# Kernel tuning notes

Hardware: AMD Instinct MI355X
Metric: run time of the kernel (lower is better)

Reference implementation:

```python
import jax, jax.numpy as jnp
import numpy as np
import math

D_POLY = 2  # polynomial order d
N_NODES = 50000
IN_FEATS = 128
H_FEATS = 64
N_EDGES = 800000


def calc_thetas(d):
    # Beta-wavelet polynomial coefficients (ascending order), matching calculate_theta2
    thetas = []
    for i in range(d + 1):
        p = np.poly1d([1.0])
        for _ in range(i):
            p = p * np.poly1d([0.5, 0.0])      # (x/2)
        for _ in range(d - i):
            p = p * np.poly1d([-0.5, 1.0])     # (1 - x/2)
        beta = math.gamma(i + 1) * math.gamma(d + 1 - i) / math.gamma(d + 2)
        p = p / beta
        asc = p.coeffs[::-1]                   # ascending coefficients
        asc = np.concatenate([asc, np.zeros(d + 1 - len(asc))])
        thetas.append(asc.astype(np.float32))
    return thetas

THETAS = calc_thetas(D_POLY)


def setup_inputs() -> dict:
    key = jax.random.key(0)
    ks = jax.random.split(key, 7)
    features = jax.random.normal(ks[0], (N_NODES, IN_FEATS), dtype=jnp.float32)
    src = jax.random.randint(ks[1], (N_EDGES,), 0, N_NODES)
    dst = jax.random.randint(ks[2], (N_EDGES,), 0, N_NODES)
    s1 = 1.0 / math.sqrt(IN_FEATS)
    W1 = jax.random.uniform(ks[3], (H_FEATS, IN_FEATS), jnp.float32, -s1, s1)
    b1 = jnp.zeros((H_FEATS,), jnp.float32)
    s2 = 1.0 / math.sqrt(H_FEATS * (D_POLY + 1))
    W2 = jax.random.uniform(ks[4], (H_FEATS, H_FEATS * (D_POLY + 1)), jnp.float32, -s2, s2)
    b2 = jnp.zeros((H_FEATS,), jnp.float32)
    return {"features": features, "src": src, "dst": dst,
            "W1": W1, "b1": b1, "W2": W2, "b2": b2}


def reference(features, src, dst, W1, b1, W2, b2):
    N = features.shape[0]
    # linear1 + ReLU
    x = jax.nn.relu(features @ W1.T + b1)  # [N, H]
    # D^{-1/2} from in-degrees (clamped at 1)
    deg = jax.ops.segment_sum(jnp.ones_like(dst, dtype=x.dtype), dst, num_segments=N)
    D_invsqrt = jnp.clip(deg, 1.0, None) ** -0.5  # [N]
    D_invsqrt = D_invsqrt[:, None]

    def unn_laplacian(f):
        # f - D^{-1/2} A D^{-1/2} f   (aggregation onto destination nodes)
        agg = jax.ops.segment_sum((f * D_invsqrt)[src], dst, num_segments=N)
        return f - agg * D_invsqrt

    outs = []
    for theta in THETAS:
        f = x
        h = theta[0] * x
        for k in range(1, len(theta)):
            f = unn_laplacian(f)
            h = h + theta[k] * f
        outs.append(h)
    feats_final = jnp.concatenate(outs, axis=-1)  # [N, H*(d+1)]
    return feats_final @ W2.T + b2
```

## Files before the change

### kernel.cpp

```cpp
#include <hip/hip_runtime.h>

#define NN 50000
#define NE 800000
#define INF 128
#define HF 64
#define K2 192
#define MAXDEG 64

typedef __attribute__((ext_vector_type(8))) short short8;
typedef __attribute__((ext_vector_type(4))) float float4v;
typedef __attribute__((ext_vector_type(4))) unsigned short ushort4v;
typedef __attribute__((ext_vector_type(2))) unsigned int uint2v;

__device__ inline unsigned short f2bf(float x) {
    unsigned int u = __float_as_uint(x);
    u += 0x7FFFu + ((u >> 16) & 1u);
    return (unsigned short)(u >> 16);
}
__device__ inline float bflo(unsigned int p) { return __uint_as_float(p << 16); }
__device__ inline float bfhi(unsigned int p) { return __uint_as_float(p & 0xFFFF0000u); }


__global__ __launch_bounds__(256) void fill_ell_part(const int* __restrict__ src,
                                                     const int* __restrict__ dst,
                                                     int* __restrict__ cnt,
                                                     unsigned short* __restrict__ ell) {
    int chunk = blockIdx.x >> 3;
    int p     = blockIdx.x & 7;
    int e0 = (chunk * 256 + (int)threadIdx.x) * 4;
    if (e0 >= NE) return;
    int4 d4 = *reinterpret_cast<const int4*>(dst + e0);
    int dd[4] = {d4.x, d4.y, d4.z, d4.w};
#pragma unroll
    for (int j = 0; j < 4; ++j) {
        int d = dd[j];
        if (d / 6250 == p) {
            int pos = atomicAdd(&cnt[d], 1);
            if (pos < MAXDEG) ell[d * MAXDEG + pos] = (unsigned short)src[e0 + j];
        }
    }
}


__global__ void pack_b(const float* __restrict__ W1, const float* __restrict__ W2,
                       unsigned short* __restrict__ Bp1, unsigned short* __restrict__ Bp2,
                       int* __restrict__ cnt,
                       unsigned short* __restrict__ hb0, unsigned short* __restrict__ hb1) {
    int gid = blockIdx.x * 256 + threadIdx.x;
    for (int z = gid; z < NN; z += 20480) cnt[z] = 0;
    if (gid < HF) {
        hb0[(size_t)NN * HF + gid] = 0;
        hb1[(size_t)NN * HF + gid] = 0;
    }
    if (gid >= 20480) return;
    if (gid < 8192) {
        int j  = gid & 7;
        int l  = (gid >> 3) & 63;
        int nt = (gid >> 9) & 3;
        int kc = gid >> 11;
        int n = nt * 16 + (l & 15);
        int k = kc * 32 + (l >> 4) * 8 + j;
        Bp1[gid] = f2bf(W1[n * INF + k]);
    } else {
        int g = gid - 8192;
        int j  = g & 7;
        int l  = (g >> 3) & 63;
        int nt = (g >> 9) & 3;
        int kc = g >> 11;
        int n = nt * 16 + (l & 15);
        int k = kc * 32 + (l >> 4) * 8 + j;
        const float* row = W2 + (size_t)n * K2;
        float v;
        if (k < 64) {
            v = 3.0f * row[k];
        } else if (k < 128) {
            int c = k - 64;
            v = -3.0f * row[c] + 3.0f * row[64 + c];
        } else {
            int c = k - 128;
            v = 0.75f * row[c] - 1.5f * row[64 + c] + 0.75f * row[128 + c];
        }
        Bp2[g] = f2bf(v);
    }
}


__global__ __launch_bounds__(256) void gemm1_mfma(const float* __restrict__ F,
                                                  const unsigned short* __restrict__ Bp,
                                                  const float* __restrict__ b1,
                                                  const int* __restrict__ cnt,
                                                  unsigned short* __restrict__ xb,
                                                  unsigned short* __restrict__ hb0) {
    int tid  = threadIdx.x;
    int lane = tid & 63;
    int wv   = tid >> 6;
    int m0   = blockIdx.x * 64 + wv * 16;
    if (m0 >= NN) return;
    int mrow = lane & 15;
    int q    = lane >> 4;

    float4v acc[4];
#pragma unroll
    for (int nt = 0; nt < 4; ++nt) acc[nt] = (float4v){0.f, 0.f, 0.f, 0.f};

    const float* arow = F + (size_t)(m0 + mrow) * INF + q * 8;
#pragma unroll
    for (int kc = 0; kc < INF / 32; ++kc) {
        const float* ap = arow + kc * 32;
        float4v a0 = *reinterpret_cast<const float4v*>(ap);
        float4v a1 = *reinterpret_cast<const float4v*>(ap + 4);
        short8 af;
        af[0] = (short)f2bf(a0[0]); af[1] = (short)f2bf(a0[1]);
        af[2] = (short)f2bf(a0[2]); af[3] = (short)f2bf(a0[3]);
        af[4] = (short)f2bf(a1[0]); af[5] = (short)f2bf(a1[1]);
        af[6] = (short)f2bf(a1[2]); af[7] = (short)f2bf(a1[3]);
#pragma unroll
        for (int nt = 0; nt < 4; ++nt) {
            short8 bf = *reinterpret_cast<const short8*>(Bp + (((kc * 4 + nt) * 64 + lane) << 3));
            acc[nt] = __builtin_amdgcn_mfma_f32_16x16x32_bf16(af, bf, acc[nt], 0, 0, 0);
        }
    }

    float dn[4];
#pragma unroll
    for (int r = 0; r < 4; ++r) {
        int c = cnt[m0 + q * 4 + r];
        c = c > MAXDEG ? MAXDEG : c;
        dn[r] = rsqrtf((float)(c < 1 ? 1 : c));
    }

#pragma unroll
    for (int nt = 0; nt < 4; ++nt) {
        int n = nt * 16 + mrow;
        float bv = b1[n];
#pragma unroll
        for (int r = 0; r < 4; ++r) {
            int node = m0 + q * 4 + r;
            float v = acc[nt][r] + bv;
            v = v > 0.0f ? v : 0.0f;
            xb [(size_t)node * HF + n] = f2bf(v);
            hb0[(size_t)node * HF + n] = f2bf(v * dn[r]);
        }
    }
}


__device__ inline void gather_accum(const uint2v* __restrict__ hbd,
                                    int s0, int s1, int s2, int s3,
                                    int wmax, int base, int jj,
                                    float& e0, float& e1, float& e2, float& e3) {
    float a0=0,a1=0,a2=0,a3=0;
    float b0=0,b1=0,b2=0,b3=0;
    float c0=0,c1=0,c2=0,c3=0;
    float d0=0,d1=0,d2=0,d3=0;
    for (int k = 0; k < wmax; k += 8) {
        int o = base + (k >> 2);
        int t0 = __shfl(s0, o), t1 = __shfl(s1, o);
        int t2 = __shfl(s2, o), t3 = __shfl(s3, o);
        uint2v p0 = hbd[(size_t)t0 * 16 + jj];
        uint2v p1 = hbd[(size_t)t1 * 16 + jj];
        uint2v p2 = hbd[(size_t)t2 * 16 + jj];
        uint2v p3 = hbd[(size_t)t3 * 16 + jj];
        if (k + 4 < wmax) {
            int u0 = __shfl(s0, o + 1), u1 = __shfl(s1, o + 1);
            int u2 = __shfl(s2, o + 1), u3 = __shfl(s3, o + 1);
            uint2v q0 = hbd[(size_t)u0 * 16 + jj];
            uint2v q1 = hbd[(size_t)u1 * 16 + jj];
            uint2v q2 = hbd[(size_t)u2 * 16 + jj];
            uint2v q3 = hbd[(size_t)u3 * 16 + jj];
            a0 += bflo(q0[0]); a1 += bfhi(q0[0]); a2 += bflo(q0[1]); a3 += bfhi(q0[1]);
            b0 += bflo(q1[0]); b1 += bfhi(q1[0]); b2 += bflo(q1[1]); b3 += bfhi(q1[1]);
            c0 += bflo(q2[0]); c1 += bfhi(q2[0]); c2 += bflo(q2[1]); c3 += bfhi(q2[1]);
            d0 += bflo(q3[0]); d1 += bfhi(q3[0]); d2 += bflo(q3[1]); d3 += bfhi(q3[1]);
        }
        a0 += bflo(p0[0]); a1 += bfhi(p0[0]); a2 += bflo(p0[1]); a3 += bfhi(p0[1]);
        b0 += bflo(p1[0]); b1 += bfhi(p1[0]); b2 += bflo(p1[1]); b3 += bfhi(p1[1]);
        c0 += bflo(p2[0]); c1 += bfhi(p2[0]); c2 += bflo(p2[1]); c3 += bfhi(p2[1]);
        d0 += bflo(p3[0]); d1 += bfhi(p3[0]); d2 += bflo(p3[1]); d3 += bfhi(p3[1]);
    }
    e0 = (a0 + b0) + (c0 + d0);
    e1 = (a1 + b1) + (c1 + d1);
    e2 = (a2 + b2) + (c2 + d2);
    e3 = (a3 + b3) + (c3 + d3);
}


__global__ __launch_bounds__(256) void gather_quad(const unsigned short* __restrict__ ell,
                                                   const int* __restrict__ cnt,
                                                   const unsigned short* __restrict__ fin,
                                                   const unsigned short* __restrict__ hb,
                                                   unsigned short* __restrict__ fout,
                                                   unsigned short* __restrict__ hout) {
    int lane  = threadIdx.x & 63;
    int wv    = threadIdx.x >> 6;
    int which = lane >> 4;
    int jj    = lane & 15;
    int n = blockIdx.x * 16 + wv * 4 + which;
    int deg = cnt[n];
    deg = deg > MAXDEG ? MAXDEG : deg;

    ushort4v ids = *reinterpret_cast<const ushort4v*>(ell + (size_t)n * MAXDEG + jj * 4);
    int slot = jj * 4;
    int s0 = (slot + 0 < deg) ? (int)ids[0] : NN;
    int s1 = (slot + 1 < deg) ? (int)ids[1] : NN;
    int s2 = (slot + 2 < deg) ? (int)ids[2] : NN;
    int s3 = (slot + 3 < deg) ? (int)ids[3] : NN;

    int wmax = deg;
    wmax = max(wmax, __shfl_xor(wmax, 16));
    wmax = max(wmax, __shfl_xor(wmax, 32));

    float e0, e1, e2, e3;
    gather_accum((const uint2v*)hb, s0, s1, s2, s3, wmax, which * 16, jj, e0, e1, e2, e3);

    float dn = rsqrtf((float)(deg < 1 ? 1 : deg));

    uint2v xv = ((const uint2v*)fin)[(size_t)n * 16 + jj];
    float f0 = bflo(xv[0]) - e0 * dn;
    float f1 = bfhi(xv[0]) - e1 * dn;
    float f2 = bflo(xv[1]) - e2 * dn;
    float f3 = bfhi(xv[1]) - e3 * dn;
    uint2v ov;
    ov[0] = (unsigned int)f2bf(f0) | ((unsigned int)f2bf(f1) << 16);
    ov[1] = (unsigned int)f2bf(f2) | ((unsigned int)f2bf(f3) << 16);
    ((uint2v*)fout)[(size_t)n * 16 + jj] = ov;
    uint2v hv;
    hv[0] = (unsigned int)f2bf(f0 * dn) | ((unsigned int)f2bf(f1 * dn) << 16);
    hv[1] = (unsigned int)f2bf(f2 * dn) | ((unsigned int)f2bf(f3 * dn) << 16);
    ((uint2v*)hout)[(size_t)n * 16 + jj] = hv;
}


__global__ __launch_bounds__(256) void gather_gemm2(const unsigned short* __restrict__ ell,
                                                    const int* __restrict__ cnt,
                                                    const unsigned short* __restrict__ xb,
                                                    const unsigned short* __restrict__ f1b,
                                                    const unsigned short* __restrict__ hb1,
                                                    const unsigned short* __restrict__ Bp,
                                                    const float* __restrict__ b2,
                                                    float* __restrict__ out) {
    __shared__ __align__(16) unsigned int f2l[4][16 * 68];
    int tid  = threadIdx.x;
    int lane = tid & 63;
    int wv   = tid >> 6;
    int nb   = blockIdx.x * 64 + wv * 16;
    if (nb >= NN) return;
    unsigned int* myl = f2l[wv];

    int which = lane >> 4;
    int jj    = lane & 15;
    const uint2v* hbd = (const uint2v*)hb1;

#pragma unroll
    for (int q = 0; q < 4; ++q) {
        int n = nb + q * 4 + which;
        int deg = cnt[n];
        deg = deg > MAXDEG ? MAXDEG : deg;
        ushort4v ids = *reinterpret_cast<const ushort4v*>(ell + (size_t)n * MAXDEG + jj * 4);
        int slot = jj * 4;
        int s0 = (slot + 0 < deg) ? (int)ids[0] : NN;
        int s1 = (slot + 1 < deg) ? (int)ids[1] : NN;
        int s2 = (slot + 2 < deg) ? (int)ids[2] : NN;
        int s3 = (slot + 3 < deg) ? (int)ids[3] : NN;
        int wmax = deg;
        wmax = max(wmax, __shfl_xor(wmax, 16));
        wmax = max(wmax, __shfl_xor(wmax, 32));

        float e0, e1, e2, e3;
        gather_accum(hbd, s0, s1, s2, s3, wmax, which * 16, jj, e0, e1, e2, e3);

        float dn = rsqrtf((float)(deg < 1 ? 1 : deg));
        uint2v xv = ((const uint2v*)f1b)[(size_t)n * 16 + jj];
        float f0 = bflo(xv[0]) - e0 * dn;
        float f1 = bfhi(xv[0]) - e1 * dn;
        float f2 = bflo(xv[1]) - e2 * dn;
        float f3 = bfhi(xv[1]) - e3 * dn;
        int row = q * 4 + which;
        myl[row * 68 + jj * 2]     = (unsigned int)f2bf(f0) | ((unsigned int)f2bf(f1) << 16);
        myl[row * 68 + jj * 2 + 1] = (unsigned int)f2bf(f2) | ((unsigned int)f2bf(f3) << 16);
    }

    int mrow = lane & 15;
    int qq   = lane >> 4;
    float4v acc[4];
#pragma unroll
    for (int nt = 0; nt < 4; ++nt) acc[nt] = (float4v){0.f, 0.f, 0.f, 0.f};

    const unsigned short* ax  = xb  + (size_t)(nb + mrow) * HF + qq * 8;
    const unsigned short* a1p = f1b + (size_t)(nb + mrow) * HF + qq * 8;

#pragma unroll
    for (int kc = 0; kc < 6; ++kc) {
        short8 af;
        if (kc < 2)      af = *reinterpret_cast<const short8*>(ax + kc * 32);
        else if (kc < 4) af = *reinterpret_cast<const short8*>(a1p + (kc - 2) * 32);
        else             af = *reinterpret_cast<const short8*>(myl + mrow * 68 + (kc - 4) * 16 + qq * 4);
#pragma unroll
        for (int nt = 0; nt < 4; ++nt) {
            short8 bf = *reinterpret_cast<const short8*>(Bp + (((kc * 4 + nt) * 64 + lane) << 3));
            acc[nt] = __builtin_amdgcn_mfma_f32_16x16x32_bf16(af, bf, acc[nt], 0, 0, 0);
        }
    }

#pragma unroll
    for (int nt = 0; nt < 4; ++nt) {
        int n2 = nt * 16 + mrow;
        float bv = b2[n2];
#pragma unroll
        for (int r = 0; r < 4; ++r) {
            int node = nb + qq * 4 + r;
            out[(size_t)node * HF + n2] = acc[nt][r] + bv;
        }
    }
}


extern "C" void kernel_launch(void* const* d_in, const int* in_sizes, int n_in,
                              void* d_out, int out_size, void* d_ws, size_t ws_size,
                              hipStream_t stream) {
    const float* features = (const float*)d_in[0];
    const int*   src      = (const int*)d_in[1];
    const int*   dst      = (const int*)d_in[2];
    const float* W1       = (const float*)d_in[3];
    const float* b1       = (const float*)d_in[4];
    const float* W2       = (const float*)d_in[5];
    const float* b2       = (const float*)d_in[6];
    float* out = (float*)d_out;

    unsigned short* xb  = (unsigned short*)d_ws;
    unsigned short* hb0 = xb  + (size_t)NN * HF;
    unsigned short* f1b = hb0 + (size_t)(NN + 1) * HF;
    unsigned short* hb1 = f1b + (size_t)NN * HF;
    unsigned short* Bp1 = hb1 + (size_t)(NN + 1) * HF;
    unsigned short* Bp2 = Bp1 + 8192;
    unsigned short* ell = Bp2 + 12288;
    int*   cnt  = (int*)(ell + (size_t)NN * MAXDEG);

    pack_b<<<80, 256, 0, stream>>>(W1, W2, Bp1, Bp2, cnt, hb0, hb1);

    fill_ell_part<<<((NE + 1023) / 1024) * 8, 256, 0, stream>>>(src, dst, cnt, ell);

    gemm1_mfma<<<(NN + 63) / 64, 256, 0, stream>>>(features, Bp1, b1, cnt, xb, hb0);

    gather_quad<<<NN / 16, 256, 0, stream>>>(ell, cnt, xb, hb0, f1b, hb1);

    gather_gemm2<<<(NN + 63) / 64, 256, 0, stream>>>(ell, cnt, xb, f1b, hb1, Bp2, b2, out);
}
```

Baseline: 170.5 us.

## Split gather_gemm2 into 16-node blocks with per-wave output column tiles

gather_gemm2 now gives each 256-thread block 16 nodes instead of 64. Each wave gathers one group of 4 nodes, then stages x, f1 and f2 rows in shared memory, and after a barrier each wave computes one 16-column output tile with six MFMAs. The shared gather_accum loop also drops its two-step unroll, so each iteration issues one batch of loads. The aim is more blocks, shorter per-wave serial gather chains and better latency hiding, at the cost of a __syncthreads, extra LDS staging and less memory-level parallelism per iteration in the gather.

```diff
diff --git a/kernel.cpp b/kernel.cpp
--- a/kernel.cpp
+++ b/kernel.cpp
@@ -153,7 +153,7 @@
     float b0=0,b1=0,b2=0,b3=0;
     float c0=0,c1=0,c2=0,c3=0;
     float d0=0,d1=0,d2=0,d3=0;
-    for (int k = 0; k < wmax; k += 8) {
+    for (int k = 0; k < wmax; k += 4) {
         int o = base + (k >> 2);
         int t0 = __shfl(s0, o), t1 = __shfl(s1, o);
         int t2 = __shfl(s2, o), t3 = __shfl(s3, o);
@@ -161,18 +161,6 @@
         uint2v p1 = hbd[(size_t)t1 * 16 + jj];
         uint2v p2 = hbd[(size_t)t2 * 16 + jj];
         uint2v p3 = hbd[(size_t)t3 * 16 + jj];
-        if (k + 4 < wmax) {
-            int u0 = __shfl(s0, o + 1), u1 = __shfl(s1, o + 1);
-            int u2 = __shfl(s2, o + 1), u3 = __shfl(s3, o + 1);
-            uint2v q0 = hbd[(size_t)u0 * 16 + jj];
-            uint2v q1 = hbd[(size_t)u1 * 16 + jj];
-            uint2v q2 = hbd[(size_t)u2 * 16 + jj];
-            uint2v q3 = hbd[(size_t)u3 * 16 + jj];
-            a0 += bflo(q0[0]); a1 += bfhi(q0[0]); a2 += bflo(q0[1]); a3 += bfhi(q0[1]);
-            b0 += bflo(q1[0]); b1 += bfhi(q1[0]); b2 += bflo(q1[1]); b3 += bfhi(q1[1]);
-            c0 += bflo(q2[0]); c1 += bfhi(q2[0]); c2 += bflo(q2[1]); c3 += bfhi(q2[1]);
-            d0 += bflo(q3[0]); d1 += bfhi(q3[0]); d2 += bflo(q3[1]); d3 += bfhi(q3[1]);
-        }
         a0 += bflo(p0[0]); a1 += bfhi(p0[0]); a2 += bflo(p0[1]); a3 += bfhi(p0[1]);
         b0 += bflo(p1[0]); b1 += bfhi(p1[0]); b2 += bflo(p1[1]); b3 += bfhi(p1[1]);
         c0 += bflo(p2[0]); c1 += bfhi(p2[0]); c2 += bflo(p2[1]); c3 += bfhi(p2[1]);
@@ -239,78 +227,68 @@
                                                     const unsigned short* __restrict__ Bp,
                                                     const float* __restrict__ b2,
                                                     float* __restrict__ out) {
-    __shared__ __align__(16) unsigned int f2l[4][16 * 68];
-    int tid  = threadIdx.x;
-    int lane = tid & 63;
-    int wv   = tid >> 6;
-    int nb   = blockIdx.x * 64 + wv * 16;
-    if (nb >= NN) return;
-    unsigned int* myl = f2l[wv];
-
+    __shared__ __align__(16) unsigned int xl [16 * 68];
+    __shared__ __align__(16) unsigned int f1l[16 * 68];
+    __shared__ __align__(16) unsigned int f2l[16 * 68];
+    int tid   = threadIdx.x;
+    int lane  = tid & 63;
+    int wv    = tid >> 6;
     int which = lane >> 4;
     int jj    = lane & 15;
-    const uint2v* hbd = (const uint2v*)hb1;
-
-#pragma unroll
-    for (int q = 0; q < 4; ++q) {
-        int n = nb + q * 4 + which;
-        int deg = cnt[n];
-        deg = deg > MAXDEG ? MAXDEG : deg;
-        ushort4v ids = *reinterpret_cast<const ushort4v*>(ell + (size_t)n * MAXDEG + jj * 4);
-        int slot = jj * 4;
-        int s0 = (slot + 0 < deg) ? (int)ids[0] : NN;
-        int s1 = (slot + 1 < deg) ? (int)ids[1] : NN;
-        int s2 = (slot + 2 < deg) ? (int)ids[2] : NN;
-        int s3 = (slot + 3 < deg) ? (int)ids[3] : NN;
-        int wmax = deg;
-        wmax = max(wmax, __shfl_xor(wmax, 16));
-        wmax = max(wmax, __shfl_xor(wmax, 32));
-
-        float e0, e1, e2, e3;
-        gather_accum(hbd, s0, s1, s2, s3, wmax, which * 16, jj, e0, e1, e2, e3);
-
-        float dn = rsqrtf((float)(deg < 1 ? 1 : deg));
-        uint2v xv = ((const uint2v*)f1b)[(size_t)n * 16 + jj];
-        float f0 = bflo(xv[0]) - e0 * dn;
-        float f1 = bfhi(xv[0]) - e1 * dn;
-        float f2 = bflo(xv[1]) - e2 * dn;
-        float f3 = bfhi(xv[1]) - e3 * dn;
-        int row = q * 4 + which;
-        myl[row * 68 + jj * 2]     = (unsigned int)f2bf(f0) | ((unsigned int)f2bf(f1) << 16);
-        myl[row * 68 + jj * 2 + 1] = (unsigned int)f2bf(f2) | ((unsigned int)f2bf(f3) << 16);
-    }
+    int row   = wv * 4 + which;
+    int n     = blockIdx.x * 16 + row;
+
+    int deg = cnt[n];
+    deg = deg > MAXDEG ? MAXDEG : deg;
+    ushort4v ids = *reinterpret_cast<const ushort4v*>(ell + (size_t)n * MAXDEG + jj * 4);
+    int slot = jj * 4;
+    int s0 = (slot + 0 < deg) ? (int)ids[0] : NN;
+    int s1 = (slot + 1 < deg) ? (int)ids[1] : NN;
+    int s2 = (slot + 2 < deg) ? (int)ids[2] : NN;
+    int s3 = (slot + 3 < deg) ? (int)ids[3] : NN;
+    int wmax = deg;
+    wmax = max(wmax, __shfl_xor(wmax, 16));
+    wmax = max(wmax, __shfl_xor(wmax, 32));
+
+    float e0, e1, e2, e3;
+    gather_accum((const uint2v*)hb1, s0, s1, s2, s3, wmax, which * 16, jj, e0, e1, e2, e3);
+
+    float dn = rsqrtf((float)(deg < 1 ? 1 : deg));
+    uint2v xv  = ((const uint2v*)f1b)[(size_t)n * 16 + jj];
+    uint2v xbv = ((const uint2v*)xb )[(size_t)n * 16 + jj];
+    float f0 = bflo(xv[0]) - e0 * dn;
+    float f1 = bfhi(xv[0]) - e1 * dn;
+    float f2 = bflo(xv[1]) - e2 * dn;
+    float f3 = bfhi(xv[1]) - e3 * dn;
+
+    int o = row * 68 + jj * 2;
+    xl [o] = xbv[0]; xl [o + 1] = xbv[1];
+    f1l[o] = xv[0];  f1l[o + 1] = xv[1];
+    f2l[o]     = (unsigned int)f2bf(f0) | ((unsigned int)f2bf(f1) << 16);
+    f2l[o + 1] = (unsigned int)f2bf(f2) | ((unsigned int)f2bf(f3) << 16);
+
+    __syncthreads();
 
     int mrow = lane & 15;
     int qq   = lane >> 4;
-    float4v acc[4];
-#pragma unroll
-    for (int nt = 0; nt < 4; ++nt) acc[nt] = (float4v){0.f, 0.f, 0.f, 0.f};
-
-    const unsigned short* ax  = xb  + (size_t)(nb + mrow) * HF + qq * 8;
-    const unsigned short* a1p = f1b + (size_t)(nb + mrow) * HF + qq * 8;
+    float4v acc = (float4v){0.f, 0.f, 0.f, 0.f};
 
 #pragma unroll
     for (int kc = 0; kc < 6; ++kc) {
-        short8 af;
-        if (kc < 2)      af = *reinterpret_cast<const short8*>(ax + kc * 32);
-        else if (kc < 4) af = *reinterpret_cast<const short8*>(a1p + (kc - 2) * 32);
-        else             af = *reinterpret_cast<const short8*>(myl + mrow * 68 + (kc - 4) * 16 + qq * 4);
-#pragma unroll
-        for (int nt = 0; nt < 4; ++nt) {
-            short8 bf = *reinterpret_cast<const short8*>(Bp + (((kc * 4 + nt) * 64 + lane) << 3));
-            acc[nt] = __builtin_amdgcn_mfma_f32_16x16x32_bf16(af, bf, acc[nt], 0, 0, 0);
-        }
-    }
-
-#pragma unroll
-    for (int nt = 0; nt < 4; ++nt) {
-        int n2 = nt * 16 + mrow;
-        float bv = b2[n2];
-#pragma unroll
-        for (int r = 0; r < 4; ++r) {
-            int node = nb + qq * 4 + r;
-            out[(size_t)node * HF + n2] = acc[nt][r] + bv;
-        }
+        const unsigned int* srcT = (kc < 2) ? xl : (kc < 4) ? f1l : f2l;
+        int kk = kc & 1;
+        short8 af = *reinterpret_cast<const short8*>(srcT + mrow * 68 + kk * 16 + qq * 4);
+        short8 bf = *reinterpret_cast<const short8*>(Bp + (((kc * 4 + wv) * 64 + lane) << 3));
+        acc = __builtin_amdgcn_mfma_f32_16x16x32_bf16(af, bf, acc, 0, 0, 0);
+    }
+
+    int n2 = wv * 16 + mrow;
+    float bv = b2[n2];
+    int nb = blockIdx.x * 16;
+#pragma unroll
+    for (int r = 0; r < 4; ++r) {
+        int node = nb + qq * 4 + r;
+        out[(size_t)node * HF + n2] = acc[r] + bv;
     }
 }
 
@@ -344,5 +322,5 @@
 
     gather_quad<<<NN / 16, 256, 0, stream>>>(ell, cnt, xb, hb0, f1b, hb1);
 
-    gather_gemm2<<<(NN + 63) / 64, 256, 0, stream>>>(ell, cnt, xb, f1b, hb1, Bp2, b2, out);
-}
+    gather_gemm2<<<NN / 16, 256, 0, stream>>>(ell, cnt, xb, f1b, hb1, Bp2, b2, out);
+}
```

Result: faster. 166.9 us (-2.1%).
